# Performance work log

Measured on AMD Instinct MI355X. Metric: run time of the kernel, lower is better.

Reference implementation:

```python
import jax, jax.numpy as jnp
import numpy as np

EMBED_DIM = 2048
NUM_HEADS = 16
HEAD_DIM = EMBED_DIM // NUM_HEADS
B, T = 4, 2048


def setup_inputs() -> dict:
    key = jax.random.key(0)
    ks = jax.random.split(key, 9)
    s = 1.0 / np.sqrt(EMBED_DIM)
    x = jax.random.normal(ks[0], (B, T, EMBED_DIM), dtype=jnp.float32)
    Wq = jax.random.normal(ks[1], (EMBED_DIM, EMBED_DIM), dtype=jnp.float32) * s
    bq = jnp.zeros((EMBED_DIM,), dtype=jnp.float32)
    Wk = jax.random.normal(ks[2], (EMBED_DIM, EMBED_DIM), dtype=jnp.float32) * s
    bk = jnp.zeros((EMBED_DIM,), dtype=jnp.float32)
    Wv = jax.random.normal(ks[3], (EMBED_DIM, EMBED_DIM), dtype=jnp.float32) * s
    bv = jnp.zeros((EMBED_DIM,), dtype=jnp.float32)
    Wo = jax.random.normal(ks[4], (EMBED_DIM, EMBED_DIM), dtype=jnp.float32) * s
    bo = jnp.zeros((EMBED_DIM,), dtype=jnp.float32)
    return {"x": x, "Wq": Wq, "bq": bq, "Wk": Wk, "bk": bk,
            "Wv": Wv, "bv": bv, "Wo": Wo, "bo": bo}


def reference(x, Wq, bq, Wk, bk, Wv, bv, Wo, bo):
    Bb, Tt, C = x.shape
    H, D = NUM_HEADS, C // NUM_HEADS
    # QKV projections (Linear: x @ W.T + b), reshape to [B, H, T, D]
    q = (jnp.einsum('btc,oc->bto', x, Wq) + bq).reshape(Bb, Tt, H, D).transpose(0, 2, 1, 3)
    k = (jnp.einsum('btc,oc->bto', x, Wk) + bk).reshape(Bb, Tt, H, D).transpose(0, 2, 1, 3)
    v = (jnp.einsum('btc,oc->bto', x, Wv) + bv).reshape(Bb, Tt, H, D).transpose(0, 2, 1, 3)
    logits = jnp.einsum('bhqd,bhkd->bhqk', q, k) / jnp.sqrt(jnp.float32(D))
    causal = jnp.triu(jnp.ones((Tt, Tt), dtype=bool), 1)  # True above diagonal
    logits = jnp.where(causal, -jnp.inf, logits)
    attn = jax.nn.softmax(logits, axis=-1)
    out = jnp.einsum('bhqk,bhkd->bhqd', attn, v)  # [B, H, T, D]
    out = out.transpose(0, 2, 1, 3).reshape(Bb, Tt, C)
    y = jnp.einsum('btc,oc->bto', out, Wo) + bo
    return y
```

## Files before the change

### kernel.cpp

```cpp
#include <hip/hip_runtime.h>
#include <hip/hip_bf16.h>
#include <cstdint>
#include <cstddef>

typedef __attribute__((ext_vector_type(8))) short short8;
typedef __attribute__((ext_vector_type(4))) short short4_;
typedef __attribute__((ext_vector_type(4))) float floatx4;
typedef __attribute__((ext_vector_type(4))) unsigned short ushort4_;

#define MFMA16(a, b, c) __builtin_amdgcn_mfma_f32_16x16x32_bf16((a), (b), (c), 0, 0, 0)

__device__ __forceinline__ unsigned short f2bf(float f) {
  __hip_bfloat16 h = __float2bfloat16(f);
  return *reinterpret_cast<unsigned short*>(&h);
}

__device__ __forceinline__ float exp2_fast(float x) {
  float r;
  asm("v_exp_f32 %0, %1" : "=v"(r) : "v"(x));
  return r;
}

__device__ __forceinline__ void gl_lds16(const void* g, void* lds) {
  __builtin_amdgcn_global_load_lds(
      (const __attribute__((address_space(1))) void*)g,
      (__attribute__((address_space(3))) void*)lds, 16, 0, 0);
}

__global__ void cast5_f32_bf16(const float* __restrict__ x, const float* __restrict__ wq,
                               const float* __restrict__ wk, const float* __restrict__ wv,
                               const float* __restrict__ wo,
                               __hip_bfloat16* __restrict__ xb, __hip_bfloat16* __restrict__ wqb,
                               __hip_bfloat16* __restrict__ wkb, __hip_bfloat16* __restrict__ wvb,
                               __hip_bfloat16* __restrict__ wob) {
  const int bid = blockIdx.x;
  const float* src;
  __hip_bfloat16* dst;
  int base;
  if (bid < 16384)      { src = x;  dst = xb;  base = bid; }
  else if (bid < 20480) { src = wq; dst = wqb; base = bid - 16384; }
  else if (bid < 24576) { src = wk; dst = wkb; base = bid - 20480; }
  else if (bid < 28672) { src = wv; dst = wvb; base = bid - 24576; }
  else                  { src = wo; dst = wob; base = bid - 28672; }
  const int i = base * 1024 + threadIdx.x * 4;
  const float4 v = *reinterpret_cast<const float4*>(src + i);
  ushort4_ o = { f2bf(v.x), f2bf(v.y), f2bf(v.z), f2bf(v.w) };
  *reinterpret_cast<ushort4_*>(dst + i) = o;
}

template <int MODE>
__global__ __launch_bounds__(512, 2)
void gemm256q(const __hip_bfloat16* __restrict__ Ap, const __hip_bfloat16* __restrict__ Bp,
              const float* __restrict__ bias, void* __restrict__ Cout,
              int M, int N, int K) {
  __shared__ __align__(16) __hip_bfloat16 SA[2][256 * 64];
  __shared__ __align__(16) __hip_bfloat16 SB[2][256 * 64];

  const int tid = threadIdx.x;
  const int wid = tid >> 6, lane = tid & 63;
  const int wr = wid >> 2, wc = wid & 3;
  const int g = lane >> 4, c16 = lane & 15;

  const int nbn = N >> 8;
  const int cpx = gridDim.x >> 3;
  const int swzb = (blockIdx.x & 7) * cpx + (blockIdx.x >> 3);
  const int bm = swzb / nbn, bn = swzb % nbn;

  const int srow8 = lane >> 3;
  const int sc8 = lane & 7;
  const int sgcol = (sc8 ^ srow8) * 8;

  floatx4 acc[8][4] = {};
  short8 af[4], bf[4];

  auto stageA = [&](int p, int kt, int slot) {
    const int ck = p * 8 + wid;
    const int row = ck * 8 + srow8;
    gl_lds16(Ap + (size_t)(bm * 256 + row) * K + kt * 64 + sgcol, SA[slot] + ck * 512);
  };
  auto stageB = [&](int p, int kt, int slot) {
    const int ck = p * 8 + wid;
    const int row = ck * 8 + srow8;
    gl_lds16(Bp + (size_t)(bn * 256 + row) * K + kt * 64 + sgcol, SB[slot] + ck * 512);
  };
  auto readA = [&](int slot, int mh, int kk) {
    const __hip_bfloat16* sa = SA[slot];
#pragma unroll
    for (int mi = 0; mi < 4; ++mi)
      af[mi] = *reinterpret_cast<const short8*>(
          sa + (wr * 128 + (mh * 4 + mi) * 16 + c16) * 64 + (((kk * 4 + g) ^ (c16 & 7)) * 8));
  };
  auto readB = [&](int slot, int kk) {
    const __hip_bfloat16* sb = SB[slot];
#pragma unroll
    for (int n = 0; n < 4; ++n)
      bf[n] = *reinterpret_cast<const short8*>(
          sb + (wc * 64 + n * 16 + c16) * 64 + (((kk * 4 + g) ^ (c16 & 7)) * 8));
  };
  auto mfma_q = [&](int mh) {
    __builtin_amdgcn_s_setprio(1);
#pragma unroll
    for (int mi = 0; mi < 4; ++mi)
#pragma unroll
      for (int n = 0; n < 4; ++n)
        acc[mh * 4 + mi][n] = MFMA16(af[mi], bf[n], acc[mh * 4 + mi][n]);
    __builtin_amdgcn_s_setprio(0);
  };

  const int nkt = K >> 6;
#pragma unroll
  for (int p = 0; p < 4; ++p) { stageA(p, 0, 0); stageB(p, 0, 0); }
  asm volatile("s_waitcnt vmcnt(0)" ::: "memory");
  __builtin_amdgcn_s_barrier();

  for (int kt = 0; kt < nkt; ++kt) {
    const int s = kt & 1;
    const bool hn = (kt + 1 < nkt);
    readA(s, 0, 0);
    readB(s, 0);
    if (hn) { stageA(0, kt + 1, s ^ 1); stageB(0, kt + 1, s ^ 1);
              stageA(1, kt + 1, s ^ 1); stageB(1, kt + 1, s ^ 1); }
    __builtin_amdgcn_s_barrier();
    mfma_q(0);
    __builtin_amdgcn_s_barrier();
    readA(s, 1, 0);
    if (hn) { stageA(2, kt + 1, s ^ 1); stageB(2, kt + 1, s ^ 1);
              stageA(3, kt + 1, s ^ 1); stageB(3, kt + 1, s ^ 1); }
    __builtin_amdgcn_s_barrier();
    mfma_q(1);
    __builtin_amdgcn_s_barrier();
    readA(s, 0, 1);
    readB(s, 1);
    __builtin_amdgcn_s_barrier();
    mfma_q(0);
    __builtin_amdgcn_s_barrier();
    readA(s, 1, 1);
    __builtin_amdgcn_s_barrier();
    mfma_q(1);
    if (hn) asm volatile("s_waitcnt vmcnt(0)" ::: "memory");
    __builtin_amdgcn_s_barrier();
  }

#pragma unroll
  for (int n = 0; n < 4; ++n) {
    const int colg = bn * 256 + wc * 64 + n * 16 + c16;
    const float bv = bias[colg];
#pragma unroll
    for (int m = 0; m < 8; ++m) {
      const int rowg = bm * 256 + wr * 128 + m * 16 + g * 4;
      if (MODE == 0) {
        __hip_bfloat16* C = (__hip_bfloat16*)Cout;
#pragma unroll
        for (int j = 0; j < 4; ++j)
          C[(size_t)(rowg + j) * N + colg] = __float2bfloat16(acc[m][n][j] + bv);
      } else if (MODE == 1) {
        __hip_bfloat16* C = (__hip_bfloat16*)Cout;
        const int bb = rowg >> 11, t0 = rowg & 2047;
        ushort4_ pk = { f2bf(acc[m][n][0] + bv), f2bf(acc[m][n][1] + bv),
                        f2bf(acc[m][n][2] + bv), f2bf(acc[m][n][3] + bv) };
        *reinterpret_cast<ushort4_*>(C + ((size_t)bb * 2048 + colg) * 2048 + t0) = pk;
      } else {
        float* C = (float*)Cout;
#pragma unroll
        for (int j = 0; j < 4; ++j)
          C[(size_t)(rowg + j) * N + colg] = acc[m][n][j] + bv;
      }
    }
  }
}

__global__ __launch_bounds__(256, 2)
void attn_fwd12(const __hip_bfloat16* __restrict__ Q, const __hip_bfloat16* __restrict__ K,
                const __hip_bfloat16* __restrict__ Vt, __hip_bfloat16* __restrict__ ctx) {
  constexpr int T = 2048, C = 2048, D = 128;
  __shared__ __align__(16) __hip_bfloat16 Ks[64 * 128];
  __shared__ __align__(16) __hip_bfloat16 Vs[128 * 64];
  __shared__ __align__(16) __hip_bfloat16 Pl[4][16 * 64];

  const int tid = threadIdx.x;
  const int w = tid >> 6, lane = tid & 63;
  const int g = lane >> 4, c16 = lane & 15;

  const int bid = blockIdx.x;
  const int x = bid & 7;
  const int i = bid >> 3;
  const int lo = i & 3, hi = i >> 5;
  const int bh = x * 8 + ((i >> 2) & 7);
  const int qb = (int)((0xF12C4A97865B3DE0ull >> (4 * (hi * 4 + lo))) & 15);
  const int b = bh >> 4, h = bh & 15;
  const int wq = qb * 128 + w * 32;

  const __hip_bfloat16* Qh = Q + (size_t)b * T * C + h * D;
  const __hip_bfloat16* Kh = K + (size_t)b * T * C + h * D;
  const __hip_bfloat16* Vh = Vt + (size_t)bh * D * T;

  const float scale2 = 0.12751744f;

  short8 qf[2][4];
#pragma unroll
  for (int m = 0; m < 2; ++m)
#pragma unroll
    for (int kk = 0; kk < 4; ++kk) {
      short8 v = *reinterpret_cast<const short8*>(Qh + (size_t)(wq + m * 16 + c16) * C + kk * 32 + g * 8);
      short8 r;
#pragma unroll
      for (int e = 0; e < 8; ++e) {
        unsigned short u = (unsigned short)v[e];
        __hip_bfloat16 bh16 = *reinterpret_cast<__hip_bfloat16*>(&u);
        r[e] = (short)f2bf(__bfloat162float(bh16) * scale2);
      }
      qf[m][kk] = r;
    }

  floatx4 acc[2][8] = {};
  float mrow[2] = {-INFINITY, -INFINITY};
  float lrow[2] = {0.f, 0.f};

  const int krow = tid >> 4;
  const int kslot = (tid & 15) ^ (krow & 7);
  const int kgcol = (tid & 15) * 8;
  const int vrow = tid >> 3;
  const int vslot = (tid & 7) ^ (vrow & 7);
  const int vgcol = (tid & 7) * 8;

  short8 kr[4], vr[4];
  auto gloadK = [&](int kb) {
#pragma unroll
    for (int p = 0; p < 4; ++p)
      kr[p] = *reinterpret_cast<const short8*>(Kh + (size_t)(kb + p * 16 + krow) * C + kgcol);
  };
  auto gloadV = [&](int kb) {
#pragma unroll
    for (int p = 0; p < 4; ++p)
      vr[p] = *reinterpret_cast<const short8*>(Vh + (size_t)(p * 32 + vrow) * T + kb + vgcol);
  };

  __hip_bfloat16* Pq = Pl[w];
  const int nkt = qb * 2 + 2;
  gloadK(0);
  gloadV(0);

  for (int kt = 0; kt < nkt; ++kt) {
    const int kb = kt * 64;
    __syncthreads();
#pragma unroll
    for (int p = 0; p < 4; ++p)
      *reinterpret_cast<short8*>(&Ks[(p * 16 + krow) * 128 + kslot * 8]) = kr[p];
#pragma unroll
    for (int p = 0; p < 4; ++p)
      *reinterpret_cast<short8*>(&Vs[(p * 32 + vrow) * 64 + vslot * 8]) = vr[p];
    __syncthreads();

    const bool hasnext = (kt + 1 < nkt);
    const bool part = (kb <= wq + 31);
    if (hasnext) gloadK(kb + 64);

    short8 pb[2][2];
    if (part) {
      floatx4 s[2][4] = {};
      __builtin_amdgcn_s_setprio(1);
#pragma unroll
      for (int n = 0; n < 4; ++n)
#pragma unroll
        for (int kk = 0; kk < 4; ++kk) {
          short8 kf = *reinterpret_cast<const short8*>(
              &Ks[(n * 16 + c16) * 128 + (((kk * 4 + g) ^ (c16 & 7)) * 8)]);
          s[0][n] = MFMA16(kf, qf[0][kk], s[0][n]);
          s[1][n] = MFMA16(kf, qf[1][kk], s[1][n]);
        }
      __builtin_amdgcn_s_setprio(0);

      const bool needmask = (kb + 63 > wq);
      float vmax[2];
      if (needmask) {
#pragma unroll
        for (int m = 0; m < 2; ++m) {
          const int q = wq + m * 16 + c16;
          float vm = -INFINITY;
#pragma unroll
          for (int n = 0; n < 4; ++n)
#pragma unroll
            for (int j = 0; j < 4; ++j) {
              float a = s[m][n][j];
              if (kb + n * 16 + g * 4 + j > q) a = -INFINITY;
              s[m][n][j] = a;
              vm = fmaxf(vm, a);
            }
          vmax[m] = vm;
        }
      } else {
#pragma unroll
        for (int m = 0; m < 2; ++m) {
          float v0 = fmaxf(fmaxf(s[m][0][0], s[m][0][1]), fmaxf(s[m][0][2], s[m][0][3]));
          float v1 = fmaxf(fmaxf(s[m][1][0], s[m][1][1]), fmaxf(s[m][1][2], s[m][1][3]));
          float v2 = fmaxf(fmaxf(s[m][2][0], s[m][2][1]), fmaxf(s[m][2][2], s[m][2][3]));
          float v3 = fmaxf(fmaxf(s[m][3][0], s[m][3][1]), fmaxf(s[m][3][2], s[m][3][3]));
          vmax[m] = fmaxf(fmaxf(v0, v1), fmaxf(v2, v3));
        }
      }
#pragma unroll
      for (int m = 0; m < 2; ++m) {
        vmax[m] = fmaxf(vmax[m], __shfl_xor(vmax[m], 16));
        vmax[m] = fmaxf(vmax[m], __shfl_xor(vmax[m], 32));
      }
      const float grow = fmaxf(vmax[0] - mrow[0], vmax[1] - mrow[1]);
      const bool nore = __all(grow <= 8.0f);
#pragma unroll
      for (int m = 0; m < 2; ++m) {
        const float mn = nore ? mrow[m] : fmaxf(mrow[m], vmax[m]);
        float rs = 0.f;
#pragma unroll
        for (int n = 0; n < 4; ++n) {
          float p0 = exp2_fast(s[m][n][0] - mn), p1 = exp2_fast(s[m][n][1] - mn);
          float p2 = exp2_fast(s[m][n][2] - mn), p3 = exp2_fast(s[m][n][3] - mn);
          rs += (p0 + p1) + (p2 + p3);
          ushort4_ pk = { f2bf(p0), f2bf(p1), f2bf(p2), f2bf(p3) };
          *reinterpret_cast<ushort4_*>(&Pq[c16 * 64 + (((4 * n + g) ^ c16) * 4)]) = pk;
        }
        rs += __shfl_xor(rs, 16);
        rs += __shfl_xor(rs, 32);
        if (nore) {
          lrow[m] += rs;
        } else {
          const float sc = exp2_fast(mrow[m] - mn);
          lrow[m] = lrow[m] * sc + rs;
          mrow[m] = mn;
#pragma unroll
          for (int dt = 0; dt < 8; ++dt)
#pragma unroll
            for (int j = 0; j < 4; ++j) acc[m][dt][j] *= sc;
        }
#pragma unroll
        for (int ks = 0; ks < 2; ++ks) {
          short4_ lo2 = *reinterpret_cast<const short4_*>(&Pq[c16 * 64 + (((8 * ks + 2 * g) ^ c16) * 4)]);
          short4_ hi2 = *reinterpret_cast<const short4_*>(&Pq[c16 * 64 + (((8 * ks + 2 * g + 1) ^ c16) * 4)]);
          short8 r;
          r[0] = lo2[0]; r[1] = lo2[1]; r[2] = lo2[2]; r[3] = lo2[3];
          r[4] = hi2[0]; r[5] = hi2[1]; r[6] = hi2[2]; r[7] = hi2[3];
          pb[m][ks] = r;
        }
      }
    }
    if (hasnext) gloadV(kb + 64);
    if (part) {
      __builtin_amdgcn_s_setprio(1);
#pragma unroll
      for (int dt = 0; dt < 8; ++dt)
#pragma unroll
        for (int ks = 0; ks < 2; ++ks) {
          const int pslot = ((ks * 4 + g) ^ (c16 & 7)) * 8;
          short8 vf = *reinterpret_cast<const short8*>(&Vs[(dt * 16 + c16) * 64 + pslot]);
          acc[0][dt] = MFMA16(vf, pb[0][ks], acc[0][dt]);
          acc[1][dt] = MFMA16(vf, pb[1][ks], acc[1][dt]);
        }
      __builtin_amdgcn_s_setprio(0);
    }
  }

#pragma unroll
  for (int m = 0; m < 2; ++m) {
    const float inv = 1.0f / lrow[m];
    const size_t row = (size_t)b * T + wq + m * 16 + c16;
#pragma unroll
    for (int dt = 0; dt < 8; ++dt) {
      ushort4_ o = { f2bf(acc[m][dt][0] * inv), f2bf(acc[m][dt][1] * inv),
                     f2bf(acc[m][dt][2] * inv), f2bf(acc[m][dt][3] * inv) };
      *reinterpret_cast<ushort4_*>(ctx + row * C + h * D + dt * 16 + g * 4) = o;
    }
  }
}

extern "C" void kernel_launch(void* const* d_in, const int* in_sizes, int n_in,
                              void* d_out, int out_size, void* d_ws, size_t ws_size,
                              hipStream_t stream) {
  const float* x  = (const float*)d_in[0];
  const float* Wq = (const float*)d_in[1];
  const float* bq = (const float*)d_in[2];
  const float* Wk = (const float*)d_in[3];
  const float* bk = (const float*)d_in[4];
  const float* Wv = (const float*)d_in[5];
  const float* bv = (const float*)d_in[6];
  const float* Wo = (const float*)d_in[7];
  const float* bo = (const float*)d_in[8];

  const int M = 8192, N = 2048, K = 2048;
  const size_t MB = 1u << 20;
  char* ws = (char*)d_ws;
  __hip_bfloat16* xb  = (__hip_bfloat16*)(ws);
  __hip_bfloat16* wqb = (__hip_bfloat16*)(ws + 32 * MB);
  __hip_bfloat16* wkb = (__hip_bfloat16*)(ws + 40 * MB);
  __hip_bfloat16* wvb = (__hip_bfloat16*)(ws + 48 * MB);
  __hip_bfloat16* wob = (__hip_bfloat16*)(ws + 56 * MB);
  __hip_bfloat16* Qb  = (__hip_bfloat16*)(ws + 64 * MB);
  __hip_bfloat16* Kb  = (__hip_bfloat16*)(ws + 96 * MB);
  __hip_bfloat16* Vtb = (__hip_bfloat16*)(ws + 128 * MB);
  if (ws_size < 160 * MB) return;

  cast5_f32_bf16<<<32768, 256, 0, stream>>>(x, Wq, Wk, Wv, Wo, xb, wqb, wkb, wvb, wob);

  const dim3 gg((M / 256) * (N / 256));
  gemm256q<0><<<gg, 512, 0, stream>>>(xb, wqb, bq, Qb, M, N, K);
  gemm256q<0><<<gg, 512, 0, stream>>>(xb, wkb, bk, Kb, M, N, K);
  gemm256q<1><<<gg, 512, 0, stream>>>(xb, wvb, bv, Vtb, M, N, K);

  attn_fwd12<<<64 * 16, 256, 0, stream>>>(Qb, Kb, Vtb, xb);

  gemm256q<2><<<gg, 512, 0, stream>>>(xb, wob, bo, d_out, M, N, K);
}
```

Baseline: 440.4 us.

## Restructure GEMM main loop to single barrier and vectorize epilogue stores

The GEMM K-loop now issues all next-tile global-to-LDS staging up front and runs the four LDS-read/MFMA quarters back to back with one barrier per iteration instead of eight. For the row-major output modes, the MFMA operands are swapped so each lane holds four consecutive columns, which allows 4-wide vectorized bias loads and packed bf16/float4 stores in place of scalar strided writes. This cuts synchronization overhead and store instruction count, but it changes how LDS reads interleave with the async loads and MFMAs.

```diff
diff --git a/kernel.cpp b/kernel.cpp
--- a/kernel.cpp
+++ b/kernel.cpp
@@ -50,9 +50,10 @@
 
 template <int MODE>
 __global__ __launch_bounds__(512, 2)
-void gemm256q(const __hip_bfloat16* __restrict__ Ap, const __hip_bfloat16* __restrict__ Bp,
+void gemm256r(const __hip_bfloat16* __restrict__ Ap, const __hip_bfloat16* __restrict__ Bp,
               const float* __restrict__ bias, void* __restrict__ Cout,
               int M, int N, int K) {
+  constexpr bool SW = (MODE != 1);
   __shared__ __align__(16) __hip_bfloat16 SA[2][256 * 64];
   __shared__ __align__(16) __hip_bfloat16 SB[2][256 * 64];
 
@@ -103,7 +104,8 @@
     for (int mi = 0; mi < 4; ++mi)
 #pragma unroll
       for (int n = 0; n < 4; ++n)
-        acc[mh * 4 + mi][n] = MFMA16(af[mi], bf[n], acc[mh * 4 + mi][n]);
+        acc[mh * 4 + mi][n] = SW ? MFMA16(bf[n], af[mi], acc[mh * 4 + mi][n])
+                                 : MFMA16(af[mi], bf[n], acc[mh * 4 + mi][n]);
     __builtin_amdgcn_s_setprio(0);
   };
 
@@ -116,54 +118,54 @@
   for (int kt = 0; kt < nkt; ++kt) {
     const int s = kt & 1;
     const bool hn = (kt + 1 < nkt);
-    readA(s, 0, 0);
+    if (hn) {
+#pragma unroll
+      for (int p = 0; p < 4; ++p) { stageA(p, kt + 1, s ^ 1); stageB(p, kt + 1, s ^ 1); }
+    }
     readB(s, 0);
-    if (hn) { stageA(0, kt + 1, s ^ 1); stageB(0, kt + 1, s ^ 1);
-              stageA(1, kt + 1, s ^ 1); stageB(1, kt + 1, s ^ 1); }
-    __builtin_amdgcn_s_barrier();
-    mfma_q(0);
-    __builtin_amdgcn_s_barrier();
-    readA(s, 1, 0);
-    if (hn) { stageA(2, kt + 1, s ^ 1); stageB(2, kt + 1, s ^ 1);
-              stageA(3, kt + 1, s ^ 1); stageB(3, kt + 1, s ^ 1); }
-    __builtin_amdgcn_s_barrier();
-    mfma_q(1);
-    __builtin_amdgcn_s_barrier();
-    readA(s, 0, 1);
+    readA(s, 0, 0); mfma_q(0);
+    readA(s, 1, 0); mfma_q(1);
     readB(s, 1);
-    __builtin_amdgcn_s_barrier();
-    mfma_q(0);
-    __builtin_amdgcn_s_barrier();
-    readA(s, 1, 1);
-    __builtin_amdgcn_s_barrier();
-    mfma_q(1);
+    readA(s, 0, 1); mfma_q(0);
+    readA(s, 1, 1); mfma_q(1);
     if (hn) asm volatile("s_waitcnt vmcnt(0)" ::: "memory");
     __builtin_amdgcn_s_barrier();
   }
 
-#pragma unroll
-  for (int n = 0; n < 4; ++n) {
-    const int colg = bn * 256 + wc * 64 + n * 16 + c16;
-    const float bv = bias[colg];
+  if (SW) {
 #pragma unroll
     for (int m = 0; m < 8; ++m) {
-      const int rowg = bm * 256 + wr * 128 + m * 16 + g * 4;
-      if (MODE == 0) {
-        __hip_bfloat16* C = (__hip_bfloat16*)Cout;
-#pragma unroll
-        for (int j = 0; j < 4; ++j)
-          C[(size_t)(rowg + j) * N + colg] = __float2bfloat16(acc[m][n][j] + bv);
-      } else if (MODE == 1) {
+      const int rowg = bm * 256 + wr * 128 + m * 16 + c16;
+#pragma unroll
+      for (int n = 0; n < 4; ++n) {
+        const int colb = bn * 256 + wc * 64 + n * 16 + g * 4;
+        const float4 b4 = *reinterpret_cast<const float4*>(bias + colb);
+        if (MODE == 0) {
+          __hip_bfloat16* C = (__hip_bfloat16*)Cout;
+          ushort4_ pk = { f2bf(acc[m][n][0] + b4.x), f2bf(acc[m][n][1] + b4.y),
+                          f2bf(acc[m][n][2] + b4.z), f2bf(acc[m][n][3] + b4.w) };
+          *reinterpret_cast<ushort4_*>(C + (size_t)rowg * N + colb) = pk;
+        } else {
+          float* C = (float*)Cout;
+          float4 st = { acc[m][n][0] + b4.x, acc[m][n][1] + b4.y,
+                        acc[m][n][2] + b4.z, acc[m][n][3] + b4.w };
+          *reinterpret_cast<float4*>(C + (size_t)rowg * N + colb) = st;
+        }
+      }
+    }
+  } else {
+#pragma unroll
+    for (int n = 0; n < 4; ++n) {
+      const int colg = bn * 256 + wc * 64 + n * 16 + c16;
+      const float bv = bias[colg];
+#pragma unroll
+      for (int m = 0; m < 8; ++m) {
+        const int rowg = bm * 256 + wr * 128 + m * 16 + g * 4;
         __hip_bfloat16* C = (__hip_bfloat16*)Cout;
         const int bb = rowg >> 11, t0 = rowg & 2047;
         ushort4_ pk = { f2bf(acc[m][n][0] + bv), f2bf(acc[m][n][1] + bv),
                         f2bf(acc[m][n][2] + bv), f2bf(acc[m][n][3] + bv) };
         *reinterpret_cast<ushort4_*>(C + ((size_t)bb * 2048 + colg) * 2048 + t0) = pk;
-      } else {
-        float* C = (float*)Cout;
-#pragma unroll
-        for (int j = 0; j < 4; ++j)
-          C[(size_t)(rowg + j) * N + colg] = acc[m][n][j] + bv;
       }
     }
   }
@@ -399,11 +401,11 @@
   cast5_f32_bf16<<<32768, 256, 0, stream>>>(x, Wq, Wk, Wv, Wo, xb, wqb, wkb, wvb, wob);
 
   const dim3 gg((M / 256) * (N / 256));
-  gemm256q<0><<<gg, 512, 0, stream>>>(xb, wqb, bq, Qb, M, N, K);
-  gemm256q<0><<<gg, 512, 0, stream>>>(xb, wkb, bk, Kb, M, N, K);
-  gemm256q<1><<<gg, 512, 0, stream>>>(xb, wvb, bv, Vtb, M, N, K);
+  gemm256r<0><<<gg, 512, 0, stream>>>(xb, wqb, bq, Qb, M, N, K);
+  gemm256r<0><<<gg, 512, 0, stream>>>(xb, wkb, bk, Kb, M, N, K);
+  gemm256r<1><<<gg, 512, 0, stream>>>(xb, wvb, bv, Vtb, M, N, K);
 
   attn_fwd12<<<64 * 16, 256, 0, stream>>>(Qb, Kb, Vtb, xb);
 
-  gemm256q<2><<<gg, 512, 0, stream>>>(xb, wob, bo, d_out, M, N, K);
-}
+  gemm256r<2><<<gg, 512, 0, stream>>>(xb, wob, bo, d_out, M, N, K);
+}
```

Measured after the change: 449.1 us. Within noise of the previous version (+2.0%).

## Halve attention query tile to 64 rows with 2-wave blocks and remove GEMM setprio

Applied to the files above, without the earlier changes.

The attention kernel now uses 128-thread blocks, each handling 64 query rows, with twice as many blocks (2048). The query blocks are paired in a simple light/heavy interleaved order instead of a lookup table, so causal work is balanced across CUs. Each thread loads 8 K/V vectors per tile instead of 4, and the LDS store is moved into a helper. The GEMM's MFMA priority raise is also dropped. Smaller blocks improve load balance and occupancy, at the cost of loading each K/V tile twice as often per query row.

```diff
diff --git a/kernel.cpp b/kernel.cpp
--- a/kernel.cpp
+++ b/kernel.cpp
@@ -98,13 +98,11 @@
           sb + (wc * 64 + n * 16 + c16) * 64 + (((kk * 4 + g) ^ (c16 & 7)) * 8));
   };
   auto mfma_q = [&](int mh) {
-    __builtin_amdgcn_s_setprio(1);
 #pragma unroll
     for (int mi = 0; mi < 4; ++mi)
 #pragma unroll
       for (int n = 0; n < 4; ++n)
         acc[mh * 4 + mi][n] = MFMA16(af[mi], bf[n], acc[mh * 4 + mi][n]);
-    __builtin_amdgcn_s_setprio(0);
   };
 
   const int nkt = K >> 6;
@@ -169,13 +167,13 @@
   }
 }
 
-__global__ __launch_bounds__(256, 2)
-void attn_fwd12(const __hip_bfloat16* __restrict__ Q, const __hip_bfloat16* __restrict__ K,
+__global__ __launch_bounds__(128, 2)
+void attn_fwd13(const __hip_bfloat16* __restrict__ Q, const __hip_bfloat16* __restrict__ K,
                 const __hip_bfloat16* __restrict__ Vt, __hip_bfloat16* __restrict__ ctx) {
   constexpr int T = 2048, C = 2048, D = 128;
   __shared__ __align__(16) __hip_bfloat16 Ks[64 * 128];
   __shared__ __align__(16) __hip_bfloat16 Vs[128 * 64];
-  __shared__ __align__(16) __hip_bfloat16 Pl[4][16 * 64];
+  __shared__ __align__(16) __hip_bfloat16 Pl[2][16 * 64];
 
   const int tid = threadIdx.x;
   const int w = tid >> 6, lane = tid & 63;
@@ -184,11 +182,12 @@
   const int bid = blockIdx.x;
   const int x = bid & 7;
   const int i = bid >> 3;
-  const int lo = i & 3, hi = i >> 5;
   const int bh = x * 8 + ((i >> 2) & 7);
-  const int qb = (int)((0xF12C4A97865B3DE0ull >> (4 * (hi * 4 + lo))) & 15);
+  const int lo2 = i & 3;
+  const int t = i >> 5;
+  const int qb = (lo2 & 1) ? (2 * t + (lo2 >> 1)) : (31 - 2 * t - (lo2 >> 1));
   const int b = bh >> 4, h = bh & 15;
-  const int wq = qb * 128 + w * 32;
+  const int wq = qb * 64 + w * 32;
 
   const __hip_bfloat16* Qh = Q + (size_t)b * T * C + h * D;
   const __hip_bfloat16* Kh = K + (size_t)b * T * C + h * D;
@@ -216,39 +215,44 @@
   float mrow[2] = {-INFINITY, -INFINITY};
   float lrow[2] = {0.f, 0.f};
 
-  const int krow = tid >> 4;
-  const int kslot = (tid & 15) ^ (krow & 7);
-  const int kgcol = (tid & 15) * 8;
-  const int vrow = tid >> 3;
-  const int vslot = (tid & 7) ^ (vrow & 7);
-  const int vgcol = (tid & 7) * 8;
-
-  short8 kr[4], vr[4];
+  const int kR = tid >> 4;
+  const int kS = tid & 15;
+  const int vR = tid >> 3;
+  const int vS = tid & 7;
+
+  short8 kr[8], vr[8];
   auto gloadK = [&](int kb) {
 #pragma unroll
-    for (int p = 0; p < 4; ++p)
-      kr[p] = *reinterpret_cast<const short8*>(Kh + (size_t)(kb + p * 16 + krow) * C + kgcol);
+    for (int p = 0; p < 8; ++p)
+      kr[p] = *reinterpret_cast<const short8*>(Kh + (size_t)(kb + p * 8 + kR) * C + kS * 8);
   };
   auto gloadV = [&](int kb) {
 #pragma unroll
-    for (int p = 0; p < 4; ++p)
-      vr[p] = *reinterpret_cast<const short8*>(Vh + (size_t)(p * 32 + vrow) * T + kb + vgcol);
+    for (int p = 0; p < 8; ++p)
+      vr[p] = *reinterpret_cast<const short8*>(Vh + (size_t)(p * 16 + vR) * T + kb + vS * 8);
+  };
+  auto writeKV = [&]() {
+#pragma unroll
+    for (int p = 0; p < 8; ++p) {
+      const int row = p * 8 + kR;
+      *reinterpret_cast<short8*>(&Ks[row * 128 + ((kS ^ (row & 7)) * 8)]) = kr[p];
+    }
+#pragma unroll
+    for (int p = 0; p < 8; ++p) {
+      const int row = p * 16 + vR;
+      *reinterpret_cast<short8*>(&Vs[row * 64 + ((vS ^ (row & 7)) * 8)]) = vr[p];
+    }
   };
 
   __hip_bfloat16* Pq = Pl[w];
-  const int nkt = qb * 2 + 2;
+  const int nkt = qb + 1;
   gloadK(0);
   gloadV(0);
 
   for (int kt = 0; kt < nkt; ++kt) {
     const int kb = kt * 64;
     __syncthreads();
-#pragma unroll
-    for (int p = 0; p < 4; ++p)
-      *reinterpret_cast<short8*>(&Ks[(p * 16 + krow) * 128 + kslot * 8]) = kr[p];
-#pragma unroll
-    for (int p = 0; p < 4; ++p)
-      *reinterpret_cast<short8*>(&Vs[(p * 32 + vrow) * 64 + vslot * 8]) = vr[p];
+    writeKV();
     __syncthreads();
 
     const bool hasnext = (kt + 1 < nkt);
@@ -332,11 +336,11 @@
         }
 #pragma unroll
         for (int ks = 0; ks < 2; ++ks) {
-          short4_ lo2 = *reinterpret_cast<const short4_*>(&Pq[c16 * 64 + (((8 * ks + 2 * g) ^ c16) * 4)]);
-          short4_ hi2 = *reinterpret_cast<const short4_*>(&Pq[c16 * 64 + (((8 * ks + 2 * g + 1) ^ c16) * 4)]);
+          short4_ lo3 = *reinterpret_cast<const short4_*>(&Pq[c16 * 64 + (((8 * ks + 2 * g) ^ c16) * 4)]);
+          short4_ hi3 = *reinterpret_cast<const short4_*>(&Pq[c16 * 64 + (((8 * ks + 2 * g + 1) ^ c16) * 4)]);
           short8 r;
-          r[0] = lo2[0]; r[1] = lo2[1]; r[2] = lo2[2]; r[3] = lo2[3];
-          r[4] = hi2[0]; r[5] = hi2[1]; r[6] = hi2[2]; r[7] = hi2[3];
+          r[0] = lo3[0]; r[1] = lo3[1]; r[2] = lo3[2]; r[3] = lo3[3];
+          r[4] = hi3[0]; r[5] = hi3[1]; r[6] = hi3[2]; r[7] = hi3[3];
           pb[m][ks] = r;
         }
       }
@@ -403,7 +407,7 @@
   gemm256q<0><<<gg, 512, 0, stream>>>(xb, wkb, bk, Kb, M, N, K);
   gemm256q<1><<<gg, 512, 0, stream>>>(xb, wvb, bv, Vtb, M, N, K);
 
-  attn_fwd12<<<64 * 16, 256, 0, stream>>>(Qb, Kb, Vtb, xb);
+  attn_fwd13<<<64 * 32, 128, 0, stream>>>(Qb, Kb, Vtb, xb);
 
   gemm256q<2><<<gg, 512, 0, stream>>>(xb, wob, bo, d_out, M, N, K);
 }
```

After: 599.7 us. 1.36x slower.
